# Kernel tuning notes

Hardware: AMD Instinct MI355X
Metric: run time of the kernel (lower is better)

## Reference

```python
import jax, jax.numpy as jnp
import numpy as np

H = 132  # hidden size hard-coded in SpatialRelationLayer

def _mlp(x, w1, b1, w2, b2, w3, b3):
    # FCBlock: 2 hidden layers of width 132 with ReLU, then linear out;
    # NNNet wraps it with sigmoid(out * 5)
    h = jax.nn.relu(x @ w1 + b1)
    h = jax.nn.relu(h @ w2 + b2)
    return jax.nn.sigmoid((h @ w3 + b3) * 5.0)

def _mlp_params(key, din, dout):
    k1, k2, k3 = jax.random.split(key, 3)
    def lin(k, i, o):
        kw, kb = jax.random.split(k)
        s = 1.0 / np.sqrt(i)
        return (jax.random.uniform(kw, (i, o), jnp.float32, -s, s),
                jax.random.uniform(kb, (o,), jnp.float32, -s, s))
    w1, b1 = lin(k1, din, H)
    w2, b2 = lin(k2, H, H)
    w3, b3 = lin(k3, H, dout)
    return w1, b1, w2, b2, w3, b3

def setup_inputs() -> dict:
    key = jax.random.key(0)
    b, N, D0, D1, D2 = 8, 128, 128, 128, 64
    O0, O1, O2 = 64, 64, 64
    kP, kQ, kR, kp, kq, kr = jax.random.split(key, 6)
    inp = {
        "P": jax.random.normal(kP, (b, D0), jnp.float32),
        "Q": jax.random.normal(kQ, (b, N, D1), jnp.float32),
        "R": jax.random.normal(kR, (b, N, N, D2), jnp.float32),
    }
    for name, k, din, dout in (("p", kp, D0 + D1, O0),
                               ("q", kq, D1 + D0 + 2 * D2, O1),
                               ("r", kr, D2 + 2 * D1, O2)):
        w1, b1, w2, b2, w3, b3 = _mlp_params(k, din, dout)
        inp.update({f"{name}_w1": w1, f"{name}_b1": b1,
                    f"{name}_w2": w2, f"{name}_b2": b2,
                    f"{name}_w3": w3, f"{name}_b3": b3})
    return inp

def reference(P, Q, R,
              p_w1, p_b1, p_w2, p_b2, p_w3, p_b3,
              q_w1, q_b1, q_w2, q_b2, q_w3, q_b3,
              r_w1, r_b1, r_w2, r_b2, r_w3, r_b3):
    b, N, D1 = Q.shape
    # P branch: global max over objects, concat with P
    P_inputs = jnp.concatenate([jnp.max(Q, axis=1), P], axis=1)  # [b, D1+D0]
    P_out = _mlp(P_inputs, p_w1, p_b1, p_w2, p_b2, p_w3, p_b3)
    # Q branch: broadcast P per-object, max-reduce relations over each axis
    P_exp = jnp.broadcast_to(P[:, None, :], (b, N, P.shape[1]))  # [b,N,D0]
    R_red0 = jnp.max(R, axis=1)  # [b,N,D2]
    R_red1 = jnp.max(R, axis=2)  # [b,N,D2]
    Q_inputs = jnp.concatenate([P_exp, Q, R_red0, R_red1], axis=2)
    Q_out = _mlp(Q_inputs, q_w1, q_b1, q_w2, q_b2, q_w3, q_b3)
    # R branch: pairwise broadcast of Q along both axes, concat with R
    Q0 = jnp.broadcast_to(Q[:, None, :, :], (b, N, N, D1))  # repeat along dim 1
    Q1 = jnp.broadcast_to(Q[:, :, None, :], (b, N, N, D1))  # repeat along dim 2
    R_inputs = jnp.concatenate([R, Q0, Q1], axis=-1)  # [b,N,N,D2+2*D1]
    R_out = _mlp(R_inputs, r_w1, r_b1, r_w2, r_b2, r_w3, r_b3)
    return (P_out, Q_out, R_out)
```

## Files before the change

### kernel.cpp

```cpp
#include <hip/hip_runtime.h>

typedef _Float16 f16;
typedef f16 f16x8 __attribute__((ext_vector_type(8)));
typedef f16 f16x4 __attribute__((ext_vector_type(4)));
typedef float f32x4 __attribute__((ext_vector_type(4)));
typedef float f32x2 __attribute__((ext_vector_type(2)));
typedef unsigned u32;

#define MFMA16(a, b, c) __builtin_amdgcn_mfma_f32_16x16x32_f16(a, b, c, 0, 0, 0)

#define OFF_RW1A 0
#define OFF_RW2  10240
#define OFF_RW3  35840
#define OFF_QW1  46080
#define OFF_QW2  87040
#define OFF_QW3  112640
#define OFF_PW1  122880
#define OFF_PW2  163840
#define OFF_PW3  189440
#define PACK_BYTES 399360

#define PREP_BLOCKS 1651

struct InPtrs { const float* p[21]; };

__device__ const int g_mSrc[9] = {15, 17, 19, 9, 11, 13, 3, 5, 7};
__device__ const int g_mK0[9]  = {0, 0, 0, 128, 0, 0, 0, 0, 0};
__device__ const int g_mK[9]   = {64, 132, 132, 256, 132, 132, 256, 132, 132};
__device__ const int g_mN[9]   = {132, 132, 64, 132, 132, 64, 132, 132, 64};
__device__ const int g_mNT[9]  = {10, 10, 4, 10, 10, 4, 10, 10, 4};
__device__ const int g_mDst[9] = {OFF_RW1A, OFF_RW2, OFF_RW3, OFF_QW1, OFF_QW2, OFF_QW3,
                                  OFF_PW1, OFF_PW2, OFF_PW3};
__device__ const int g_mBlk0[9] = {256, 261, 274, 279, 299, 312, 317, 337, 350};

__global__ __launch_bounds__(256) void prep_kernel(InPtrs in, f16* __restrict__ wpk,
    float* __restrict__ c1, float* __restrict__ d1, float* __restrict__ e1q,
    float* __restrict__ qmax, float* __restrict__ red0p, float* __restrict__ red1)
{
  __shared__ float sbuf[1024];
  const int mb = blockIdx.x, t = threadIdx.x;

  if (mb < 256) {
    const int b = mb >> 5, jo = (mb >> 1) & 15, ih = mb & 1;
    const float* base = in.p[2] + (size_t)b * 1048576 + (size_t)ih * 64 * 8192
                        + (size_t)jo * 512 + t * 2;
    f32x2 m[8];
    #pragma unroll
    for (int u = 0; u < 8; ++u) { m[u][0] = -3.4e38f; m[u][1] = -3.4e38f; }
    for (int i = 0; i < 64; i += 8) {
      #pragma unroll
      for (int u = 0; u < 8; ++u) {
        f32x2 v = *(const f32x2*)(base + (size_t)(i + u) * 8192);
        m[u][0] = fmaxf(m[u][0], v[0]);
        m[u][1] = fmaxf(m[u][1], v[1]);
      }
    }
    #pragma unroll
    for (int s = 4; s > 0; s >>= 1)
      #pragma unroll
      for (int u = 0; u < 4; ++u)
        if (u < s) {
          m[u][0] = fmaxf(m[u][0], m[u + s][0]);
          m[u][1] = fmaxf(m[u][1], m[u + s][1]);
        }
    *(f32x2*)(red0p + (size_t)ih * 65536 +
              ((size_t)(b * 128 + jo * 8 + (t >> 5))) * 64 + ((t * 2) & 63)) = m[0];
  } else if (mb < 355) {
    int mi = 8;
    while (mi > 0 && mb < g_mBlk0[mi]) --mi;
    const int NT = g_mNT[mi], K = g_mK[mi], N = g_mN[mi], K0 = g_mK0[mi];
    const int L = (mb - g_mBlk0[mi]) * 256 + t;
    const int lanes = ((K + 31) >> 5) * NT * 64;
    if (L < lanes) {
      const int lane = L & 63, tile = L >> 6;
      const int kk = tile / NT, nn = tile % NT;
      const float* src = in.p[g_mSrc[mi]];
      const int n = nn * 16 + (lane & 15);
      const int kb = kk * 32 + ((lane >> 4) << 3);
      f16x8 v;
      #pragma unroll
      for (int u = 0; u < 8; ++u) {
        const int k = kb + u;
        float f = (k < K && n < N) ? src[(size_t)(K0 + k) * N + n] : 0.f;
        v[u] = (f16)f;
      }
      *(f16x8*)(wpk + g_mDst[mi] + (size_t)L * 8) = v;
    }
  } else if (mb < 363) {
    const int b = mb - 355;
    const float* Qb = in.p[1] + (size_t)b * 128 * 128;
    const int d = t & 127, g = t >> 7;
    float m0 = -3.4e38f, m1 = m0, m2 = m0, m3 = m0;
    #pragma unroll
    for (int v = 0; v < 16; ++v) {
      const int i = g * 64 + v * 4;
      m0 = fmaxf(m0, Qb[(size_t)(i + 0) * 128 + d]);
      m1 = fmaxf(m1, Qb[(size_t)(i + 1) * 128 + d]);
      m2 = fmaxf(m2, Qb[(size_t)(i + 2) * 128 + d]);
      m3 = fmaxf(m3, Qb[(size_t)(i + 3) * 128 + d]);
    }
    sbuf[g * 128 + d] = fmaxf(fmaxf(m0, m1), fmaxf(m2, m3));
    __syncthreads();
    if (t < 128) qmax[b * 128 + t] = fmaxf(sbuf[t], sbuf[128 + t]);
  } else if (mb < 371) {
    const int b = mb - 363;
    const float* P = in.p[0]; const float* qw1 = in.p[9]; const float* qb1 = in.p[10];
    if (t < 160) {
      float a = 0.f;
      if (t < 132) {
        float a0 = 0.f, a1 = 0.f, a2 = 0.f, a3 = 0.f;
        for (int k = 0; k < 128; k += 4) {
          a0 += P[b * 128 + k + 0] * qw1[(size_t)(k + 0) * 132 + t];
          a1 += P[b * 128 + k + 1] * qw1[(size_t)(k + 1) * 132 + t];
          a2 += P[b * 128 + k + 2] * qw1[(size_t)(k + 2) * 132 + t];
          a3 += P[b * 128 + k + 3] * qw1[(size_t)(k + 3) * 132 + t];
        }
        a = qb1[t] + (a0 + a1) + (a2 + a3);
      }
      e1q[b * 160 + t] = a;
    }
  } else if (mb < 627) {
    const int blk = mb - 371;
    const float* Q = in.p[1]; const float* rw1 = in.p[15]; const float* rb1 = in.p[16];
    for (int o = t; o < 512; o += 256) sbuf[o] = Q[(size_t)blk * 512 + o];
    __syncthreads();
    if (t < 160) {
      float cc[4], dd[4];
      #pragma unroll
      for (int r = 0; r < 4; ++r) { cc[r] = 0.f; dd[r] = 0.f; }
      if (t < 132) {
        const float bb = rb1[t];
        #pragma unroll
        for (int r = 0; r < 4; ++r) cc[r] = bb;
        for (int k = 0; k < 128; ++k) {
          const float wc = rw1[(size_t)(192 + k) * 132 + t];
          const float wd = rw1[(size_t)(64 + k) * 132 + t];
          #pragma unroll
          for (int r = 0; r < 4; ++r) {
            cc[r] += sbuf[r * 128 + k] * wc;
            dd[r] += sbuf[r * 128 + k] * wd;
          }
        }
      }
      for (int r = 0; r < 4; ++r) {
        c1[(size_t)(blk * 4 + r) * 160 + t] = cc[r];
        d1[(size_t)(blk * 4 + r) * 160 + t] = dd[r];
      }
    }
  } else {
    const int bi = mb - 627;
    const int d2 = t & 31, jg = t >> 5;
    const float* base = in.p[2] + (size_t)bi * 8192 + (size_t)jg * 1024 + d2 * 2;
    f32x2 m[4];
    #pragma unroll
    for (int u = 0; u < 4; ++u) { m[u][0] = -3.4e38f; m[u][1] = -3.4e38f; }
    #pragma unroll
    for (int v = 0; v < 16; v += 4) {
      #pragma unroll
      for (int u = 0; u < 4; ++u) {
        f32x2 vv = *(const f32x2*)(base + (size_t)(v + u) * 64);
        m[u][0] = fmaxf(m[u][0], vv[0]);
        m[u][1] = fmaxf(m[u][1], vv[1]);
      }
    }
    m[0][0] = fmaxf(fmaxf(m[0][0], m[1][0]), fmaxf(m[2][0], m[3][0]));
    m[0][1] = fmaxf(fmaxf(m[0][1], m[1][1]), fmaxf(m[2][1], m[3][1]));
    sbuf[jg * 64 + d2 * 2] = m[0][0];
    sbuf[jg * 64 + d2 * 2 + 1] = m[0][1];
    __syncthreads();
    if (t < 64) {
      float mm = sbuf[t];
      #pragma unroll
      for (int g2 = 1; g2 < 8; ++g2) mm = fmaxf(mm, sbuf[g2 * 64 + t]);
      red1[(size_t)bi * 64 + t] = mm;
    }
  }
}

__device__ __forceinline__ float sig5(float x) {
  return 1.f / (1.f + __expf(-5.f * x));
}

__device__ __forceinline__ u32 pk2(float a, float b) {
  typedef __fp16 fp16x2 __attribute__((ext_vector_type(2)));
  union { fp16x2 h; u32 u; } cv;
  cv.h = __builtin_amdgcn_cvt_pkrtz(a, b);
  return cv.u;
}

__device__ __forceinline__ f16x8 ld8(const float* p) {
  f32x4 v0 = *(const f32x4*)p, v1 = *(const f32x4*)(p + 4);
  union { u32 w[4]; f16x8 v; } U;
  U.w[0] = pk2(v0[0], v0[1]); U.w[1] = pk2(v0[2], v0[3]);
  U.w[2] = pk2(v1[0], v1[1]); U.w[3] = pk2(v1[2], v1[3]);
  return U.v;
}

__device__ __forceinline__ f16x8 ld8max(const float* p, int stride) {
  f32x4 a0 = *(const f32x4*)p, a1 = *(const f32x4*)(p + 4);
  f32x4 b0 = *(const f32x4*)(p + stride), b1 = *(const f32x4*)(p + stride + 4);
  union { u32 w[4]; f16x8 v; } U;
  U.w[0] = pk2(fmaxf(a0[0], b0[0]), fmaxf(a0[1], b0[1]));
  U.w[1] = pk2(fmaxf(a0[2], b0[2]), fmaxf(a0[3], b0[3]));
  U.w[2] = pk2(fmaxf(a1[0], b1[0]), fmaxf(a1[1], b1[1]));
  U.w[3] = pk2(fmaxf(a1[2], b1[2]), fmaxf(a1[3], b1[3]));
  return U.v;
}

__global__ __launch_bounds__(512, 4) void fused_kernel(
    const float* __restrict__ R, const float* __restrict__ c1, const float* __restrict__ d1,
    const float* __restrict__ rb2, const float* __restrict__ rb3,
    const f16* __restrict__ wpk, float* __restrict__ outR,
    const float* __restrict__ P, const float* __restrict__ Q,
    const float* __restrict__ qb2, const float* __restrict__ qb3,
    const float* __restrict__ pb1, const float* __restrict__ pb2, const float* __restrict__ pb3,
    const float* __restrict__ e1q, const float* __restrict__ qmax,
    const float* __restrict__ red0p, const float* __restrict__ red1,
    float* __restrict__ outP, float* __restrict__ outQ)
{
  __shared__ f16 Hs[128][168];
  const int t = threadIdx.x, lane = t & 63, w = t >> 6;
  const int wm = w >> 1, wn = w & 1;
  const int lr = (lane >> 4) << 2;
  const int lc = lane & 15;
  const int lk = (lane >> 4) << 3;
  const int rbase = wm * 32, nbase = wn * 80;
  const int blk = blockIdx.x;

  f32x4 acc[2][5];
  const f16x8 *W2p, *W3p;
  const float *b2p, *b3p;
  float* obase;
  int rowlim;

  if (blk >= 9) {
    const int bi = blk - 9;
    const int b = bi >> 7;
    const float* c1r = c1 + (size_t)bi * 160;
    const float* d1b = d1 + (size_t)b * 128 * 160;
    f32x4 cvv[5];
    #pragma unroll
    for (int n5 = 0; n5 < 5; ++n5)
      cvv[n5] = *(const f32x4*)(c1r + nbase + n5 * 16 + lr);
    #pragma unroll
    for (int mi2 = 0; mi2 < 2; ++mi2) {
      const int jl = rbase + mi2 * 16 + lc;
      const float* dr = d1b + (size_t)jl * 160 + nbase + lr;
      #pragma unroll
      for (int n5 = 0; n5 < 5; ++n5)
        acc[mi2][n5] = cvv[n5] + *(const f32x4*)(dr + n5 * 16);
    }
    const f16x8* W1p = (const f16x8*)(wpk + OFF_RW1A);
    const float* Rb = R + (size_t)bi * 8192;
    #pragma unroll
    for (int c = 0; c < 2; ++c) {
      const f16x8 a0 = ld8(Rb + (size_t)(rbase + lc) * 64 + c * 32 + lk);
      const f16x8 a1 = ld8(Rb + (size_t)(rbase + 16 + lc) * 64 + c * 32 + lk);
      #pragma unroll
      for (int n5 = 0; n5 < 5; ++n5) {
        const f16x8 bf = W1p[(size_t)(c * 10 + wn * 5 + n5) * 64 + lane];
        acc[0][n5] = MFMA16(bf, a0, acc[0][n5]);
        acc[1][n5] = MFMA16(bf, a1, acc[1][n5]);
      }
    }
    b2p = rb2; b3p = rb3;
    W2p = (const f16x8*)(wpk + OFF_RW2);
    W3p = (const f16x8*)(wpk + OFF_RW3);
    obase = outR + (size_t)bi * 8192;
    rowlim = 128;
  } else {
    const bool isP = (blk == 8);
    const int b = blk;
    #pragma unroll
    for (int n5 = 0; n5 < 5; ++n5) {
      const int nb = nbase + n5 * 16 + lr;
      f32x4 cv = {0.f, 0.f, 0.f, 0.f};
      if (isP) { if (nb < 132) cv = *(const f32x4*)(pb1 + nb); }
      else cv = *(const f32x4*)(e1q + b * 160 + nb);
      acc[0][n5] = cv; acc[1][n5] = cv;
    }
    const f16x8* W1p = (const f16x8*)(wpk + (isP ? OFF_PW1 : OFF_QW1));
    #pragma unroll
    for (int c = 0; c < 8; ++c) {
      f16x8 x[2];
      #pragma unroll
      for (int mi2 = 0; mi2 < 2; ++mi2) {
        const int jl = rbase + mi2 * 16 + lc;
        if (isP) {
          const int rr = jl & 7;
          const float* s = (c < 4) ? (qmax + rr * 128 + c * 32 + lk)
                                   : (P + rr * 128 + (c - 4) * 32 + lk);
          x[mi2] = ld8(s);
        } else {
          const size_t row = (size_t)(b * 128 + jl);
          if (c < 4)      x[mi2] = ld8(Q + row * 128 + c * 32 + lk);
          else if (c < 6) x[mi2] = ld8max(red0p + row * 64 + (c - 4) * 32 + lk, 65536);
          else            x[mi2] = ld8(red1 + row * 64 + (c - 6) * 32 + lk);
        }
      }
      #pragma unroll
      for (int n5 = 0; n5 < 5; ++n5) {
        const f16x8 bf = W1p[(size_t)(c * 10 + wn * 5 + n5) * 64 + lane];
        acc[0][n5] = MFMA16(bf, x[0], acc[0][n5]);
        acc[1][n5] = MFMA16(bf, x[1], acc[1][n5]);
      }
    }
    b2p = isP ? pb2 : qb2; b3p = isP ? pb3 : qb3;
    W2p = (const f16x8*)(wpk + (isP ? OFF_PW2 : OFF_QW2));
    W3p = (const f16x8*)(wpk + (isP ? OFF_PW3 : OFF_QW3));
    obase = isP ? outP : (outQ + (size_t)b * 128 * 64);
    rowlim = isP ? 8 : 128;
  }

  #pragma unroll
  for (int mi2 = 0; mi2 < 2; ++mi2) {
    const int jl = rbase + mi2 * 16 + lc;
    #pragma unroll
    for (int n5 = 0; n5 < 5; ++n5) {
      f16x4 hv;
      #pragma unroll
      for (int r = 0; r < 4; ++r) hv[r] = (f16)fmaxf(acc[mi2][n5][r], 0.f);
      *(f16x4*)(&Hs[jl][nbase + n5 * 16 + lr]) = hv;
    }
  }
  __syncthreads();

  #pragma unroll
  for (int n5 = 0; n5 < 5; ++n5) {
    const int nb = nbase + n5 * 16 + lr;
    f32x4 bv = {0.f, 0.f, 0.f, 0.f};
    if (nb < 132) bv = *(const f32x4*)(b2p + nb);
    acc[0][n5] = bv; acc[1][n5] = bv;
  }
  #pragma unroll
  for (int kk = 0; kk < 5; ++kk) {
    const f16x8 a0 = *(const f16x8*)(&Hs[rbase + lc][kk * 32 + lk]);
    const f16x8 a1 = *(const f16x8*)(&Hs[rbase + 16 + lc][kk * 32 + lk]);
    #pragma unroll
    for (int n5 = 0; n5 < 5; ++n5) {
      const f16x8 bf = W2p[(size_t)(kk * 10 + wn * 5 + n5) * 64 + lane];
      acc[0][n5] = MFMA16(bf, a0, acc[0][n5]);
      acc[1][n5] = MFMA16(bf, a1, acc[1][n5]);
    }
  }
  __syncthreads();
  #pragma unroll
  for (int mi2 = 0; mi2 < 2; ++mi2) {
    const int jl = rbase + mi2 * 16 + lc;
    #pragma unroll
    for (int n5 = 0; n5 < 5; ++n5) {
      f16x4 hv;
      #pragma unroll
      for (int r = 0; r < 4; ++r) hv[r] = (f16)fmaxf(acc[mi2][n5][r], 0.f);
      *(f16x4*)(&Hs[jl][nbase + n5 * 16 + lr]) = hv;
    }
  }
  __syncthreads();

  f32x4 acc3[2][2];
  const int n3base = wn * 32;
  #pragma unroll
  for (int n2 = 0; n2 < 2; ++n2) {
    const f32x4 bv = *(const f32x4*)(b3p + n3base + n2 * 16 + lr);
    acc3[0][n2] = bv; acc3[1][n2] = bv;
  }
  #pragma unroll
  for (int kk = 0; kk < 5; ++kk) {
    const f16x8 a0 = *(const f16x8*)(&Hs[rbase + lc][kk * 32 + lk]);
    const f16x8 a1 = *(const f16x8*)(&Hs[rbase + 16 + lc][kk * 32 + lk]);
    #pragma unroll
    for (int n2 = 0; n2 < 2; ++n2) {
      const f16x8 bf = W3p[(size_t)(kk * 4 + wn * 2 + n2) * 64 + lane];
      acc3[0][n2] = MFMA16(bf, a0, acc3[0][n2]);
      acc3[1][n2] = MFMA16(bf, a1, acc3[1][n2]);
    }
  }
  #pragma unroll
  for (int mi2 = 0; mi2 < 2; ++mi2) {
    const int jl = rbase + mi2 * 16 + lc;
    if (jl < rowlim) {
      #pragma unroll
      for (int n2 = 0; n2 < 2; ++n2) {
        f32x4 ov;
        #pragma unroll
        for (int r = 0; r < 4; ++r) ov[r] = sig5(acc3[mi2][n2][r]);
        *(f32x4*)(obase + (size_t)jl * 64 + n3base + n2 * 16 + lr) = ov;
      }
    }
  }
}

extern "C" void kernel_launch(void* const* d_in, const int* in_sizes, int n_in,
                              void* d_out, int out_size, void* d_ws, size_t ws_size,
                              hipStream_t stream) {
  (void)in_sizes; (void)n_in; (void)out_size; (void)ws_size;
  InPtrs ip;
  for (int i = 0; i < 21; ++i) ip.p[i] = (const float*)d_in[i];

  char* ws = (char*)d_ws;
  f16* wpk = (f16*)ws;
  float* wsf = (float*)(ws + PACK_BYTES);
  float* c1 = wsf;
  float* d1 = wsf + 163840;
  float* e1q = wsf + 327680;
  float* qmax = wsf + 328960;
  float* red0p = wsf + 329984;
  float* red1 = wsf + 461056;

  float* outP = (float*)d_out;
  float* outQ = outP + 512;
  float* outR = outP + 66048;

  prep_kernel<<<dim3(PREP_BLOCKS), dim3(256), 0, stream>>>(ip, wpk, c1, d1, e1q, qmax,
                                                           red0p, red1);
  fused_kernel<<<dim3(1033), dim3(512), 0, stream>>>((const float*)d_in[2], c1, d1,
      (const float*)d_in[18], (const float*)d_in[20], wpk, outR,
      (const float*)d_in[0], (const float*)d_in[1],
      (const float*)d_in[12], (const float*)d_in[14],
      (const float*)d_in[4], (const float*)d_in[6], (const float*)d_in[8],
      e1q, qmax, red0p, red1, outP, outQ);
}
```

Measured before the change: 69.50 us.

## Split fused blocks to 64 rows and prefetch layer weights into registers

Each fused-kernel block now handles 64 rows with 256 threads instead of 128 rows with 512 threads, so the grid doubles to 2065 blocks and the shared hidden buffer halves. Layer-2 and layer-3 weight fragments, plus the R-branch layer-1 weights and inputs, are loaded into registers early so their global-load latency overlaps with layer-1 work. Launch bounds are relaxed to (256,1) to give the register-resident weights room. In exchange, weights are re-fetched by twice as many blocks and higher register use may lower occupancy.

```diff
diff --git a/kernel.cpp b/kernel.cpp
--- a/kernel.cpp
+++ b/kernel.cpp
@@ -207,7 +207,7 @@
   return U.v;
 }
 
-__global__ __launch_bounds__(512, 4) void fused_kernel(
+__global__ __launch_bounds__(256, 1) void fused_kernel(
     const float* __restrict__ R, const float* __restrict__ c1, const float* __restrict__ d1,
     const float* __restrict__ rb2, const float* __restrict__ rb3,
     const f16* __restrict__ wpk, float* __restrict__ outR,
@@ -218,7 +218,7 @@
     const float* __restrict__ red0p, const float* __restrict__ red1,
     float* __restrict__ outP, float* __restrict__ outQ)
 {
-  __shared__ f16 Hs[128][168];
+  __shared__ f16 Hs[64][168];
   const int t = threadIdx.x, lane = t & 63, w = t >> 6;
   const int wm = w >> 1, wn = w & 1;
   const int lr = (lane >> 4) << 2;
@@ -228,16 +228,42 @@
   const int blk = blockIdx.x;
 
   f32x4 acc[2][5];
-  const f16x8 *W2p, *W3p;
+  f16x8 w2b[5][5];
+  f16x8 w3b[5][2];
+  const f16x8 *W3p;
   const float *b2p, *b3p;
   float* obase;
   int rowlim;
 
-  if (blk >= 9) {
-    const int bi = blk - 9;
+  if (blk >= 17) {
+    const int idx = blk - 17;
+    const int bi = idx >> 1, half = idx & 1;
+    const int jbase = half * 64;
     const int b = bi >> 7;
+    const float* Rb = R + (size_t)bi * 8192 + (size_t)jbase * 64;
+
+    const f16x8* W1p = (const f16x8*)(wpk + OFF_RW1A);
+    f16x8 w1b[2][5];
+    #pragma unroll
+    for (int kk = 0; kk < 2; ++kk)
+      #pragma unroll
+      for (int n5 = 0; n5 < 5; ++n5)
+        w1b[kk][n5] = W1p[(size_t)(kk * 10 + wn * 5 + n5) * 64 + lane];
+    f16x8 af[2][2];
+    #pragma unroll
+    for (int kk = 0; kk < 2; ++kk) {
+      af[kk][0] = ld8(Rb + (size_t)(rbase + lc) * 64 + kk * 32 + lk);
+      af[kk][1] = ld8(Rb + (size_t)(rbase + 16 + lc) * 64 + kk * 32 + lk);
+    }
+    const f16x8* W2p = (const f16x8*)(wpk + OFF_RW2);
+    #pragma unroll
+    for (int kk = 0; kk < 5; ++kk)
+      #pragma unroll
+      for (int n5 = 0; n5 < 5; ++n5)
+        w2b[kk][n5] = W2p[(size_t)(kk * 10 + wn * 5 + n5) * 64 + lane];
+
     const float* c1r = c1 + (size_t)bi * 160;
-    const float* d1b = d1 + (size_t)b * 128 * 160;
+    const float* d1b = d1 + ((size_t)(b * 128 + jbase)) * 160;
     f32x4 cvv[5];
     #pragma unroll
     for (int n5 = 0; n5 < 5; ++n5)
@@ -250,27 +276,31 @@
       for (int n5 = 0; n5 < 5; ++n5)
         acc[mi2][n5] = cvv[n5] + *(const f32x4*)(dr + n5 * 16);
     }
-    const f16x8* W1p = (const f16x8*)(wpk + OFF_RW1A);
-    const float* Rb = R + (size_t)bi * 8192;
-    #pragma unroll
-    for (int c = 0; c < 2; ++c) {
-      const f16x8 a0 = ld8(Rb + (size_t)(rbase + lc) * 64 + c * 32 + lk);
-      const f16x8 a1 = ld8(Rb + (size_t)(rbase + 16 + lc) * 64 + c * 32 + lk);
+    #pragma unroll
+    for (int kk = 0; kk < 2; ++kk)
       #pragma unroll
       for (int n5 = 0; n5 < 5; ++n5) {
-        const f16x8 bf = W1p[(size_t)(c * 10 + wn * 5 + n5) * 64 + lane];
-        acc[0][n5] = MFMA16(bf, a0, acc[0][n5]);
-        acc[1][n5] = MFMA16(bf, a1, acc[1][n5]);
-      }
-    }
+        acc[0][n5] = MFMA16(w1b[kk][n5], af[kk][0], acc[0][n5]);
+        acc[1][n5] = MFMA16(w1b[kk][n5], af[kk][1], acc[1][n5]);
+      }
     b2p = rb2; b3p = rb3;
-    W2p = (const f16x8*)(wpk + OFF_RW2);
     W3p = (const f16x8*)(wpk + OFF_RW3);
-    obase = outR + (size_t)bi * 8192;
-    rowlim = 128;
+    obase = outR + (size_t)bi * 8192 + (size_t)jbase * 64;
+    rowlim = 64;
   } else {
-    const bool isP = (blk == 8);
-    const int b = blk;
+    const int bs = blk;
+    const bool isP = (bs == 16);
+    const int b = bs >> 1, x0 = (bs & 1) * 64;
+    const f16x8* W1p = (const f16x8*)(wpk + (isP ? OFF_PW1 : OFF_QW1));
+    const f16x8 zz = {0, 0, 0, 0, 0, 0, 0, 0};
+
+    const f16x8* W2p = (const f16x8*)(wpk + (isP ? OFF_PW2 : OFF_QW2));
+    #pragma unroll
+    for (int kk = 0; kk < 5; ++kk)
+      #pragma unroll
+      for (int n5 = 0; n5 < 5; ++n5)
+        w2b[kk][n5] = W2p[(size_t)(kk * 10 + wn * 5 + n5) * 64 + lane];
+
     #pragma unroll
     for (int n5 = 0; n5 < 5; ++n5) {
       const int nb = nbase + n5 * 16 + lr;
@@ -279,38 +309,52 @@
       else cv = *(const f32x4*)(e1q + b * 160 + nb);
       acc[0][n5] = cv; acc[1][n5] = cv;
     }
-    const f16x8* W1p = (const f16x8*)(wpk + (isP ? OFF_PW1 : OFF_QW1));
-    #pragma unroll
-    for (int c = 0; c < 8; ++c) {
-      f16x8 x[2];
-      #pragma unroll
-      for (int mi2 = 0; mi2 < 2; ++mi2) {
-        const int jl = rbase + mi2 * 16 + lc;
+    for (int c = 0; c < 4; ++c) {
+      #pragma unroll
+      for (int kk = 0; kk < 2; ++kk) {
+        const int kq = c * 64 + kk * 32 + lk;
+        f16x8 a0 = zz, a1 = zz;
         if (isP) {
-          const int rr = jl & 7;
-          const float* s = (c < 4) ? (qmax + rr * 128 + c * 32 + lk)
-                                   : (P + rr * 128 + (c - 4) * 32 + lk);
-          x[mi2] = ld8(s);
+          #pragma unroll
+          for (int mi2 = 0; mi2 < 2; ++mi2) {
+            const int rl = rbase + mi2 * 16 + lc;
+            f16x8 av = zz;
+            if (rl < 8) {
+              const float* s = (c < 2) ? (qmax + rl * 128 + kq) : (P + rl * 128 + (kq - 128));
+              av = ld8(s);
+            }
+            if (mi2 == 0) a0 = av; else a1 = av;
+          }
         } else {
-          const size_t row = (size_t)(b * 128 + jl);
-          if (c < 4)      x[mi2] = ld8(Q + row * 128 + c * 32 + lk);
-          else if (c < 6) x[mi2] = ld8max(red0p + row * 64 + (c - 4) * 32 + lk, 65536);
-          else            x[mi2] = ld8(red1 + row * 64 + (c - 6) * 32 + lk);
+          #pragma unroll
+          for (int mi2 = 0; mi2 < 2; ++mi2) {
+            const size_t rg = (size_t)(b * 128 + x0 + rbase + mi2 * 16 + lc);
+            f16x8 av;
+            if (c < 2)          av = ld8(Q + rg * 128 + kq);
+            else if (kq < 192)  av = ld8max(red0p + rg * 64 + (kq - 128), 65536);
+            else                av = ld8(red1 + rg * 64 + (kq - 192));
+            if (mi2 == 0) a0 = av; else a1 = av;
+          }
         }
-      }
-      #pragma unroll
-      for (int n5 = 0; n5 < 5; ++n5) {
-        const f16x8 bf = W1p[(size_t)(c * 10 + wn * 5 + n5) * 64 + lane];
-        acc[0][n5] = MFMA16(bf, x[0], acc[0][n5]);
-        acc[1][n5] = MFMA16(bf, x[1], acc[1][n5]);
+        #pragma unroll
+        for (int n5 = 0; n5 < 5; ++n5) {
+          const f16x8 bf = W1p[(size_t)((c * 2 + kk) * 10 + wn * 5 + n5) * 64 + lane];
+          acc[0][n5] = MFMA16(bf, a0, acc[0][n5]);
+          acc[1][n5] = MFMA16(bf, a1, acc[1][n5]);
+        }
       }
     }
     b2p = isP ? pb2 : qb2; b3p = isP ? pb3 : qb3;
-    W2p = (const f16x8*)(wpk + (isP ? OFF_PW2 : OFF_QW2));
     W3p = (const f16x8*)(wpk + (isP ? OFF_PW3 : OFF_QW3));
-    obase = isP ? outP : (outQ + (size_t)b * 128 * 64);
-    rowlim = isP ? 8 : 128;
-  }
+    obase = isP ? outP : (outQ + ((size_t)(b * 128 + x0)) * 64);
+    rowlim = isP ? 8 : 64;
+  }
+
+  #pragma unroll
+  for (int kk = 0; kk < 5; ++kk)
+    #pragma unroll
+    for (int n2 = 0; n2 < 2; ++n2)
+      w3b[kk][n2] = W3p[(size_t)(kk * 4 + wn * 2 + n2) * 64 + lane];
 
   #pragma unroll
   for (int mi2 = 0; mi2 < 2; ++mi2) {
@@ -338,9 +382,8 @@
     const f16x8 a1 = *(const f16x8*)(&Hs[rbase + 16 + lc][kk * 32 + lk]);
     #pragma unroll
     for (int n5 = 0; n5 < 5; ++n5) {
-      const f16x8 bf = W2p[(size_t)(kk * 10 + wn * 5 + n5) * 64 + lane];
-      acc[0][n5] = MFMA16(bf, a0, acc[0][n5]);
-      acc[1][n5] = MFMA16(bf, a1, acc[1][n5]);
+      acc[0][n5] = MFMA16(w2b[kk][n5], a0, acc[0][n5]);
+      acc[1][n5] = MFMA16(w2b[kk][n5], a1, acc[1][n5]);
     }
   }
   __syncthreads();
@@ -370,9 +413,8 @@
     const f16x8 a1 = *(const f16x8*)(&Hs[rbase + 16 + lc][kk * 32 + lk]);
     #pragma unroll
     for (int n2 = 0; n2 < 2; ++n2) {
-      const f16x8 bf = W3p[(size_t)(kk * 4 + wn * 2 + n2) * 64 + lane];
-      acc3[0][n2] = MFMA16(bf, a0, acc3[0][n2]);
-      acc3[1][n2] = MFMA16(bf, a1, acc3[1][n2]);
+      acc3[0][n2] = MFMA16(w3b[kk][n2], a0, acc3[0][n2]);
+      acc3[1][n2] = MFMA16(w3b[kk][n2], a1, acc3[1][n2]);
     }
   }
   #pragma unroll
@@ -413,7 +455,7 @@
 
   prep_kernel<<<dim3(PREP_BLOCKS), dim3(256), 0, stream>>>(ip, wpk, c1, d1, e1q, qmax,
                                                            red0p, red1);
-  fused_kernel<<<dim3(1033), dim3(512), 0, stream>>>((const float*)d_in[2], c1, d1,
+  fused_kernel<<<dim3(2065), dim3(256), 0, stream>>>((const float*)d_in[2], c1, d1,
       (const float*)d_in[18], (const float*)d_in[20], wpk, outR,
       (const float*)d_in[0], (const float*)d_in[1],
       (const float*)d_in[12], (const float*)d_in[14],
```

After: 85.21 us. 22.6% more time.
